# Optimization experiments

Hardware: AMD Instinct MI355X
Metric: run time of the kernel (lower is better)

Reference implementation:

```python
import jax, jax.numpy as jnp
import numpy as np

D_MODEL = 768
NUM_HEADS = 12
D_K = D_MODEL // NUM_HEADS


def setup_inputs() -> dict:
    key = jax.random.key(0)
    ks = jax.random.split(key, 11)
    B, S, D = 2, 4096, D_MODEL
    scale = 1.0 / np.sqrt(D)
    return {
        "Q": jax.random.normal(ks[0], (B, S, D), jnp.float32),
        "K": jax.random.normal(ks[1], (B, S, D), jnp.float32),
        "V": jax.random.normal(ks[2], (B, S, D), jnp.float32),
        "Wq": jax.random.normal(ks[3], (D, D), jnp.float32) * scale,
        "bq": jnp.zeros((D,), jnp.float32),
        "Wk": jax.random.normal(ks[4], (D, D), jnp.float32) * scale,
        "bk": jnp.zeros((D,), jnp.float32),
        "Wv": jax.random.normal(ks[5], (D, D), jnp.float32) * scale,
        "bv": jnp.zeros((D,), jnp.float32),
        "Wo": jax.random.normal(ks[6], (D, D), jnp.float32) * scale,
        "bo": jnp.zeros((D,), jnp.float32),
    }


def _split_heads(x):
    # (B, S, D) -> (B, H, S, d_k)
    B, S, _ = x.shape
    return x.reshape(B, S, NUM_HEADS, D_K).transpose(0, 2, 1, 3)


def reference(Q, K, V, Wq, bq, Wk, bk, Wv, bv, Wo, bo):
    # Linear projections (torch Linear: x @ W.T + b)
    q = _split_heads(Q @ Wq.T + bq)  # (B,H,S,dk)
    k = _split_heads(K @ Wk.T + bk)
    v = _split_heads(V @ Wv.T + bv)
    # Naive unfused attention: materialize full (B,H,S,S) scores
    scores = jnp.einsum("bhqd,bhkd->bhqk", q, k) / jnp.sqrt(jnp.float32(D_K))
    probs = jax.nn.softmax(scores, axis=-1)
    attn = jnp.einsum("bhqk,bhkd->bhqd", probs, v)  # (B,H,S,dk)
    B, H, S, dk = attn.shape
    combined = attn.transpose(0, 2, 1, 3).reshape(B, S, H * dk)
    return combined @ Wo.T + bo
```

## Files before the change

### kernel.cpp

```cpp
#include <hip/hip_runtime.h>
#include <hip/hip_bf16.h>
#include <stdint.h>

#define D_MODEL 768
#define NHEAD 12
#define DK 64
#define SQ 4096
#define BATCH 2
#define MROWS (BATCH*SQ)
#define WELEMS (D_MODEL*D_MODEL)
#define XELEMS ((size_t)MROWS*D_MODEL)
#define TENS_ELEMS ((size_t)BATCH*NHEAD*SQ*DK)

#define QSCALE 0.1803368801111244f

typedef __attribute__((ext_vector_type(8))) unsigned short u16x8;
typedef __attribute__((ext_vector_type(4))) unsigned short u16x4;
typedef __attribute__((ext_vector_type(4))) unsigned int   u32x4;
typedef __attribute__((ext_vector_type(8))) __bf16 bf16x8;
typedef __attribute__((ext_vector_type(4))) float f32x4;
typedef __attribute__((ext_vector_type(16))) float f32x16;

__device__ __forceinline__ unsigned short f2bfu(float f){
    uint32_t u = __float_as_uint(f);
    return (unsigned short)((u + 0x7fffu + ((u >> 16) & 1u)) >> 16);
}

__device__ __forceinline__ bf16x8 load_bf8(const unsigned short* p){
    u16x8 t = *reinterpret_cast<const u16x8*>(p);
    return __builtin_bit_cast(bf16x8, t);
}

__device__ __forceinline__ unsigned cvtpk(float lo, float hi){
    unsigned r;
    asm("v_cvt_pk_bf16_f32 %0, %1, %2" : "=v"(r) : "v"(lo), "v"(hi));
    return r;
}

__device__ __forceinline__ f32x16 zero16(){
    f32x16 z;
    #pragma unroll
    for (int i = 0; i < 16; ++i) z[i] = 0.f;
    return z;
}

__global__ __launch_bounds__(256) void wconv_kernel(const float* w0, const float* w1,
                                                    const float* w2, const float* w3,
                                                    unsigned short* dst){
    const float* src = (blockIdx.y == 0) ? w0 : (blockIdx.y == 1) ? w1 :
                       (blockIdx.y == 2) ? w2 : w3;
    unsigned short* d = dst + (size_t)blockIdx.y * WELEMS;
    int i = (blockIdx.x * blockDim.x + threadIdx.x) * 4;
    if (i < WELEMS){
        float4 v = *reinterpret_cast<const float4*>(src + i);
        u16x4 o;
        o[0]=f2bfu(v.x); o[1]=f2bfu(v.y); o[2]=f2bfu(v.z); o[3]=f2bfu(v.w);
        *reinterpret_cast<u16x4*>(d + i) = o;
    }
}

__global__ __launch_bounds__(256) void xconv_kernel(const float* src, unsigned short* dst){
    size_t i = ((size_t)blockIdx.x * blockDim.x + threadIdx.x) * 4;
    float4 v = *reinterpret_cast<const float4*>(src + i);
    u16x4 o;
    o[0]=f2bfu(v.x); o[1]=f2bfu(v.y); o[2]=f2bfu(v.z); o[3]=f2bfu(v.w);
    *reinterpret_cast<u16x4*>(dst + i) = o;
}

template<int MODE>
__global__ __launch_bounds__(256) void gemm_kernel(const unsigned short* A, const unsigned short* Wb,
                                                   const float* bias, float oscale, void* out_){
    const int wave = threadIdx.x >> 6, lane = threadIdx.x & 63;
    const int g = lane >> 4, c16 = lane & 15;
    const int m0 = blockIdx.x * 128 + wave * 32;
    const int n0 = blockIdx.y * 64;
    f32x4 acc[2][4];
    #pragma unroll
    for (int rt = 0; rt < 2; ++rt)
        #pragma unroll
        for (int c = 0; c < 4; ++c) acc[rt][c] = f32x4{0.f,0.f,0.f,0.f};
    for (int kc = 0; kc < D_MODEL; kc += 32){
        const int kk = kc + g * 8;
        bf16x8 a0 = load_bf8(A + (size_t)(m0 + c16) * D_MODEL + kk);
        bf16x8 a1 = load_bf8(A + (size_t)(m0 + 16 + c16) * D_MODEL + kk);
        #pragma unroll
        for (int c = 0; c < 4; ++c){
            bf16x8 bfr = load_bf8(Wb + (size_t)(n0 + c*16 + c16) * D_MODEL + kk);
            acc[0][c] = __builtin_amdgcn_mfma_f32_16x16x32_bf16(a0, bfr, acc[0][c], 0, 0, 0);
            acc[1][c] = __builtin_amdgcn_mfma_f32_16x16x32_bf16(a1, bfr, acc[1][c], 0, 0, 0);
        }
    }
    #pragma unroll
    for (int rt = 0; rt < 2; ++rt){
        #pragma unroll
        for (int c = 0; c < 4; ++c){
            const int n = n0 + c*16 + c16;
            const float bv = bias[n];
            #pragma unroll
            for (int r = 0; r < 4; ++r){
                const int mrow = m0 + rt*16 + g*4 + r;
                const float v = (acc[rt][c][r] + bv) * oscale;
                if constexpr (MODE == 3){
                    ((float*)out_)[(size_t)mrow * D_MODEL + n] = v;
                } else {
                    const int b = mrow >> 12, s = mrow & 4095;
                    const int h = n >> 6, d = n & 63;
                    unsigned short* o = (unsigned short*)out_;
                    if constexpr (MODE == 2){
                        o[((size_t)(b*NHEAD + h)*DK + d)*SQ + s] = f2bfu(v);
                    } else {
                        o[((size_t)(b*NHEAD + h)*SQ + s)*DK + d] = f2bfu(v);
                    }
                }
            }
        }
    }
}

__global__ __launch_bounds__(256) void attn_kernel(const unsigned short* q, const unsigned short* k,
                                                   const unsigned short* vt, unsigned short* att){
    const int lane = threadIdx.x & 63;
    const int wave = threadIdx.x >> 6;
    const int c32 = lane & 31, hi = lane >> 5;
    const int bh = blockIdx.y;
    const int b = bh / NHEAD, h = bh % NHEAD;
    const int q0 = blockIdx.x * 128 + wave * 32;
    const unsigned short* qb = q + ((size_t)bh * SQ + q0) * DK;
    const unsigned short* kb = k + (size_t)bh * SQ * DK;
    const unsigned short* vb = vt + (size_t)bh * DK * SQ;

    bf16x8 qf[4];
    #pragma unroll
    for (int ks = 0; ks < 4; ++ks)
        qf[ks] = load_bf8(qb + (size_t)c32 * DK + ks*16 + hi*8);

    f32x16 o[2];
    o[0] = zero16(); o[1] = zero16();
    float lrow = 0.f;

    for (int kv0 = 0; kv0 < SQ; kv0 += 64){
        f32x16 sc[2];
        sc[0] = zero16(); sc[1] = zero16();
        #pragma unroll
        for (int t = 0; t < 2; ++t){
            #pragma unroll
            for (int ks = 0; ks < 4; ++ks){
                bf16x8 kf = load_bf8(kb + (size_t)(kv0 + t*32 + c32) * DK + ks*16 + hi*8);
                sc[t] = __builtin_amdgcn_mfma_f32_32x32x16_bf16(kf, qf[ks], sc[t], 0, 0, 0);
            }
        }
        float ps[16];
        #pragma unroll
        for (int r = 0; r < 16; ++r){
            float p0 = exp2f(sc[0][r]);
            float p1 = exp2f(sc[1][r]);
            sc[0][r] = p0; sc[1][r] = p1;
            ps[r] = p0 + p1;
        }
        #pragma unroll
        for (int s = 8; s > 0; s >>= 1)
            #pragma unroll
            for (int r = 0; r < 8; ++r)
                if (r < s) ps[r] += ps[r + s];
        lrow += ps[0];

        unsigned Wd[2][4][2];
        #pragma unroll
        for (int t = 0; t < 2; ++t)
            #pragma unroll
            for (int gq = 0; gq < 4; ++gq){
                Wd[t][gq][0] = cvtpk(sc[t][gq*4+0], sc[t][gq*4+1]);
                Wd[t][gq][1] = cvtpk(sc[t][gq*4+2], sc[t][gq*4+3]);
            }
        unsigned Rv[2][2][2];
        #pragma unroll
        for (int t = 0; t < 2; ++t)
            #pragma unroll
            for (int gp = 0; gp < 2; ++gp)
                #pragma unroll
                for (int w = 0; w < 2; ++w){
                    unsigned snd = hi ? Wd[t][2*gp][w] : Wd[t][2*gp+1][w];
                    Rv[t][gp][w] = (unsigned)__shfl_xor((int)snd, 32, 64);
                }
        bf16x8 paf[4];
        #pragma unroll
        for (int t = 0; t < 2; ++t)
            #pragma unroll
            for (int gp = 0; gp < 2; ++gp){
                const int f = t*2 + gp;
                u32x4 wd;
                wd[0] = hi ? Rv[t][gp][0]   : Wd[t][2*gp][0];
                wd[1] = hi ? Rv[t][gp][1]   : Wd[t][2*gp][1];
                wd[2] = hi ? Wd[t][2*gp+1][0] : Rv[t][gp][0];
                wd[3] = hi ? Wd[t][2*gp+1][1] : Rv[t][gp][1];
                paf[f] = __builtin_bit_cast(bf16x8, wd);
            }
        #pragma unroll
        for (int td = 0; td < 2; ++td){
            #pragma unroll
            for (int f = 0; f < 4; ++f){
                bf16x8 vf = load_bf8(vb + (size_t)(td*32 + c32) * SQ + kv0 + f*16 + hi*8);
                o[td] = __builtin_amdgcn_mfma_f32_32x32x16_bf16(paf[f], vf, o[td], 0, 0, 0);
            }
        }
    }

    float ltot = lrow + __shfl_xor(lrow, 32, 64);
    float linv = 1.0f / ltot;
    float li[16];
    #pragma unroll
    for (int r = 0; r < 16; ++r)
        li[r] = __shfl(linv, (r&3) + 8*(r>>2) + 4*hi, 64);
    #pragma unroll
    for (int td = 0; td < 2; ++td)
        #pragma unroll
        for (int r = 0; r < 16; ++r){
            const int qrow = (r&3) + 8*(r>>2) + 4*hi;
            att[((size_t)(b*SQ + q0 + qrow)) * D_MODEL + h*DK + td*32 + c32] =
                f2bfu(o[td][r] * li[r]);
        }
}

extern "C" void kernel_launch(void* const* d_in, const int* in_sizes, int n_in,
                              void* d_out, int out_size, void* d_ws, size_t ws_size,
                              hipStream_t stream){
    const float* Q  = (const float*)d_in[0];
    const float* K  = (const float*)d_in[1];
    const float* V  = (const float*)d_in[2];
    const float* Wq = (const float*)d_in[3];
    const float* bq = (const float*)d_in[4];
    const float* Wk = (const float*)d_in[5];
    const float* bk = (const float*)d_in[6];
    const float* Wv = (const float*)d_in[7];
    const float* bv = (const float*)d_in[8];
    const float* Wo = (const float*)d_in[9];
    const float* bo = (const float*)d_in[10];
    float* out = (float*)d_out;

    unsigned short* q_ws   = (unsigned short*)d_ws;
    unsigned short* k_ws   = q_ws  + TENS_ELEMS;
    unsigned short* vt_ws  = k_ws  + TENS_ELEMS;
    unsigned short* att_ws = vt_ws + TENS_ELEMS;
    unsigned short* wbf    = att_ws + TENS_ELEMS;
    unsigned short* xbf    = wbf + 4*WELEMS;

    wconv_kernel<<<dim3(576, 4), 256, 0, stream>>>(Wq, Wk, Wv, Wo, wbf);

    xconv_kernel<<<6144, 256, 0, stream>>>(Q, xbf);
    gemm_kernel<0><<<dim3(64, 12), 256, 0, stream>>>(xbf, wbf,            bq, QSCALE, q_ws);
    xconv_kernel<<<6144, 256, 0, stream>>>(K, xbf);
    gemm_kernel<1><<<dim3(64, 12), 256, 0, stream>>>(xbf, wbf + WELEMS,   bk, 1.0f,   k_ws);
    xconv_kernel<<<6144, 256, 0, stream>>>(V, xbf);
    gemm_kernel<2><<<dim3(64, 12), 256, 0, stream>>>(xbf, wbf + 2*WELEMS, bv, 1.0f,   vt_ws);

    attn_kernel<<<dim3(32, 24), 256, 0, stream>>>(q_ws, k_ws, vt_ws, att_ws);

    gemm_kernel<3><<<dim3(64, 12), 256, 0, stream>>>(att_ws, wbf + 3*WELEMS, bo, 1.0f, out);
}
```

Measured before the change: 693.0 us.

## Prefetch K/V fragments, use hardware exp, and halve GEMM tile rows

The attention loop now loads the K and V fragments for each 64-key block into registers ahead of the MFMAs. The second V half is issued after the score MFMAs so the loads overlap compute, and s_setprio is raised around the MFMA bursts. exp2f is replaced by the raw v_exp_f32 instruction, which drops denormal/range handling. Separately, the projection GEMM tile shrinks from 32 to 16 rows per wave with a doubled grid and pointer-increment addressing, trading A/B reuse for more blocks and lower register pressure.

```diff
diff --git a/kernel.cpp b/kernel.cpp
--- a/kernel.cpp
+++ b/kernel.cpp
@@ -34,6 +34,12 @@
 __device__ __forceinline__ unsigned cvtpk(float lo, float hi){
     unsigned r;
     asm("v_cvt_pk_bf16_f32 %0, %1, %2" : "=v"(r) : "v"(lo), "v"(hi));
+    return r;
+}
+
+__device__ __forceinline__ float exp2_hw(float x){
+    float r;
+    asm("v_exp_f32 %0, %1" : "=v"(r) : "v"(x));
     return r;
 }
 
@@ -72,45 +78,40 @@
                                                    const float* bias, float oscale, void* out_){
     const int wave = threadIdx.x >> 6, lane = threadIdx.x & 63;
     const int g = lane >> 4, c16 = lane & 15;
-    const int m0 = blockIdx.x * 128 + wave * 32;
+    const int m0 = blockIdx.x * 64 + wave * 16;
     const int n0 = blockIdx.y * 64;
-    f32x4 acc[2][4];
-    #pragma unroll
-    for (int rt = 0; rt < 2; ++rt)
-        #pragma unroll
-        for (int c = 0; c < 4; ++c) acc[rt][c] = f32x4{0.f,0.f,0.f,0.f};
+    f32x4 acc[4];
+    #pragma unroll
+    for (int c = 0; c < 4; ++c) acc[c] = f32x4{0.f,0.f,0.f,0.f};
+    const unsigned short* ap = A  + (size_t)(m0 + c16) * D_MODEL + g * 8;
+    const unsigned short* bp = Wb + (size_t)(n0 + c16) * D_MODEL + g * 8;
+    #pragma unroll 4
     for (int kc = 0; kc < D_MODEL; kc += 32){
-        const int kk = kc + g * 8;
-        bf16x8 a0 = load_bf8(A + (size_t)(m0 + c16) * D_MODEL + kk);
-        bf16x8 a1 = load_bf8(A + (size_t)(m0 + 16 + c16) * D_MODEL + kk);
+        bf16x8 af = load_bf8(ap + kc);
         #pragma unroll
         for (int c = 0; c < 4; ++c){
-            bf16x8 bfr = load_bf8(Wb + (size_t)(n0 + c*16 + c16) * D_MODEL + kk);
-            acc[0][c] = __builtin_amdgcn_mfma_f32_16x16x32_bf16(a0, bfr, acc[0][c], 0, 0, 0);
-            acc[1][c] = __builtin_amdgcn_mfma_f32_16x16x32_bf16(a1, bfr, acc[1][c], 0, 0, 0);
-        }
-    }
-    #pragma unroll
-    for (int rt = 0; rt < 2; ++rt){
-        #pragma unroll
-        for (int c = 0; c < 4; ++c){
-            const int n = n0 + c*16 + c16;
-            const float bv = bias[n];
-            #pragma unroll
-            for (int r = 0; r < 4; ++r){
-                const int mrow = m0 + rt*16 + g*4 + r;
-                const float v = (acc[rt][c][r] + bv) * oscale;
-                if constexpr (MODE == 3){
-                    ((float*)out_)[(size_t)mrow * D_MODEL + n] = v;
+            bf16x8 bfr = load_bf8(bp + (size_t)(c*16) * D_MODEL + kc);
+            acc[c] = __builtin_amdgcn_mfma_f32_16x16x32_bf16(af, bfr, acc[c], 0, 0, 0);
+        }
+    }
+    #pragma unroll
+    for (int c = 0; c < 4; ++c){
+        const int n = n0 + c*16 + c16;
+        const float bv = bias[n];
+        #pragma unroll
+        for (int r = 0; r < 4; ++r){
+            const int mrow = m0 + g*4 + r;
+            const float v = (acc[c][r] + bv) * oscale;
+            if constexpr (MODE == 3){
+                ((float*)out_)[(size_t)mrow * D_MODEL + n] = v;
+            } else {
+                const int b = mrow >> 12, s = mrow & 4095;
+                const int h = n >> 6, d = n & 63;
+                unsigned short* o = (unsigned short*)out_;
+                if constexpr (MODE == 2){
+                    o[((size_t)(b*NHEAD + h)*DK + d)*SQ + s] = f2bfu(v);
                 } else {
-                    const int b = mrow >> 12, s = mrow & 4095;
-                    const int h = n >> 6, d = n & 63;
-                    unsigned short* o = (unsigned short*)out_;
-                    if constexpr (MODE == 2){
-                        o[((size_t)(b*NHEAD + h)*DK + d)*SQ + s] = f2bfu(v);
-                    } else {
-                        o[((size_t)(b*NHEAD + h)*SQ + s)*DK + d] = f2bfu(v);
-                    }
+                    o[((size_t)(b*NHEAD + h)*SQ + s)*DK + d] = f2bfu(v);
                 }
             }
         }
@@ -126,8 +127,9 @@
     const int b = bh / NHEAD, h = bh % NHEAD;
     const int q0 = blockIdx.x * 128 + wave * 32;
     const unsigned short* qb = q + ((size_t)bh * SQ + q0) * DK;
-    const unsigned short* kb = k + (size_t)bh * SQ * DK;
-    const unsigned short* vb = vt + (size_t)bh * DK * SQ;
+
+    const unsigned short* kp = k  + (size_t)bh * SQ * DK + (size_t)c32 * DK + hi * 8;
+    const unsigned short* vp = vt + (size_t)bh * DK * SQ + (size_t)c32 * SQ + hi * 8;
 
     bf16x8 qf[4];
     #pragma unroll
@@ -138,22 +140,36 @@
     o[0] = zero16(); o[1] = zero16();
     float lrow = 0.f;
 
-    for (int kv0 = 0; kv0 < SQ; kv0 += 64){
+    for (int it = 0; it < SQ/64; ++it, kp += 64*DK, vp += 64){
+        bf16x8 kf[2][4], vf[2][4];
+        #pragma unroll
+        for (int t = 0; t < 2; ++t)
+            #pragma unroll
+            for (int ks = 0; ks < 4; ++ks)
+                kf[t][ks] = load_bf8(kp + t*32*DK + ks*16);
+        #pragma unroll
+        for (int f = 0; f < 4; ++f)
+            vf[0][f] = load_bf8(vp + f*16);
+
         f32x16 sc[2];
         sc[0] = zero16(); sc[1] = zero16();
-        #pragma unroll
-        for (int t = 0; t < 2; ++t){
-            #pragma unroll
-            for (int ks = 0; ks < 4; ++ks){
-                bf16x8 kf = load_bf8(kb + (size_t)(kv0 + t*32 + c32) * DK + ks*16 + hi*8);
-                sc[t] = __builtin_amdgcn_mfma_f32_32x32x16_bf16(kf, qf[ks], sc[t], 0, 0, 0);
-            }
-        }
+        __builtin_amdgcn_s_setprio(1);
+        #pragma unroll
+        for (int ks = 0; ks < 4; ++ks){
+            sc[0] = __builtin_amdgcn_mfma_f32_32x32x16_bf16(kf[0][ks], qf[ks], sc[0], 0, 0, 0);
+            sc[1] = __builtin_amdgcn_mfma_f32_32x32x16_bf16(kf[1][ks], qf[ks], sc[1], 0, 0, 0);
+        }
+        __builtin_amdgcn_s_setprio(0);
+
+        #pragma unroll
+        for (int f = 0; f < 4; ++f)
+            vf[1][f] = load_bf8(vp + (size_t)32*SQ + f*16);
+
         float ps[16];
         #pragma unroll
         for (int r = 0; r < 16; ++r){
-            float p0 = exp2f(sc[0][r]);
-            float p1 = exp2f(sc[1][r]);
+            float p0 = exp2_hw(sc[0][r]);
+            float p1 = exp2_hw(sc[1][r]);
             sc[0][r] = p0; sc[1][r] = p1;
             ps[r] = p0 + p1;
         }
@@ -189,20 +205,20 @@
             for (int gp = 0; gp < 2; ++gp){
                 const int f = t*2 + gp;
                 u32x4 wd;
-                wd[0] = hi ? Rv[t][gp][0]   : Wd[t][2*gp][0];
-                wd[1] = hi ? Rv[t][gp][1]   : Wd[t][2*gp][1];
+                wd[0] = hi ? Rv[t][gp][0]     : Wd[t][2*gp][0];
+                wd[1] = hi ? Rv[t][gp][1]     : Wd[t][2*gp][1];
                 wd[2] = hi ? Wd[t][2*gp+1][0] : Rv[t][gp][0];
                 wd[3] = hi ? Wd[t][2*gp+1][1] : Rv[t][gp][1];
                 paf[f] = __builtin_bit_cast(bf16x8, wd);
             }
-        #pragma unroll
-        for (int td = 0; td < 2; ++td){
-            #pragma unroll
-            for (int f = 0; f < 4; ++f){
-                bf16x8 vf = load_bf8(vb + (size_t)(td*32 + c32) * SQ + kv0 + f*16 + hi*8);
-                o[td] = __builtin_amdgcn_mfma_f32_32x32x16_bf16(paf[f], vf, o[td], 0, 0, 0);
-            }
-        }
+
+        __builtin_amdgcn_s_setprio(1);
+        #pragma unroll
+        for (int f = 0; f < 4; ++f){
+            o[0] = __builtin_amdgcn_mfma_f32_32x32x16_bf16(paf[f], vf[0][f], o[0], 0, 0, 0);
+            o[1] = __builtin_amdgcn_mfma_f32_32x32x16_bf16(paf[f], vf[1][f], o[1], 0, 0, 0);
+        }
+        __builtin_amdgcn_s_setprio(0);
     }
 
     float ltot = lrow + __shfl_xor(lrow, 32, 64);
@@ -247,13 +263,13 @@
     wconv_kernel<<<dim3(576, 4), 256, 0, stream>>>(Wq, Wk, Wv, Wo, wbf);
 
     xconv_kernel<<<6144, 256, 0, stream>>>(Q, xbf);
-    gemm_kernel<0><<<dim3(64, 12), 256, 0, stream>>>(xbf, wbf,            bq, QSCALE, q_ws);
+    gemm_kernel<0><<<dim3(128, 12), 256, 0, stream>>>(xbf, wbf,            bq, QSCALE, q_ws);
     xconv_kernel<<<6144, 256, 0, stream>>>(K, xbf);
-    gemm_kernel<1><<<dim3(64, 12), 256, 0, stream>>>(xbf, wbf + WELEMS,   bk, 1.0f,   k_ws);
+    gemm_kernel<1><<<dim3(128, 12), 256, 0, stream>>>(xbf, wbf + WELEMS,   bk, 1.0f,   k_ws);
     xconv_kernel<<<6144, 256, 0, stream>>>(V, xbf);
-    gemm_kernel<2><<<dim3(64, 12), 256, 0, stream>>>(xbf, wbf + 2*WELEMS, bv, 1.0f,   vt_ws);
+    gemm_kernel<2><<<dim3(128, 12), 256, 0, stream>>>(xbf, wbf + 2*WELEMS, bv, 1.0f,   vt_ws);
 
     attn_kernel<<<dim3(32, 24), 256, 0, stream>>>(q_ws, k_ws, vt_ws, att_ws);
 
-    gemm_kernel<3><<<dim3(64, 12), 256, 0, stream>>>(att_ws, wbf + 3*WELEMS, bo, 1.0f, out);
-}
+    gemm_kernel<3><<<dim3(128, 12), 256, 0, stream>>>(att_ws, wbf + 3*WELEMS, bo, 1.0f, out);
+}
```

After: 807.1 us. 16.5% more time.
